# Kernel optimization log

Measured on AMD Instinct MI355X. Metric: run time of the kernel, lower is better.

## Reference

```python
import jax, jax.numpy as jnp
import numpy as np

B, H, S, E = 1, 32, 2048, 512  # batch, num_heads (also head dim), seq, embed
NEG_INF = -1.0e9


def setup_inputs() -> dict:
    key = jax.random.key(0)
    ks = jax.random.split(key, 9)
    query = jax.random.normal(ks[0], (B, H, S, E), dtype=jnp.float32)
    key_t = jax.random.normal(ks[1], (B, H, S, E), dtype=jnp.float32)
    value = jax.random.normal(ks[2], (B, H, S, E), dtype=jnp.float32)
    mask = jax.random.randint(ks[3], (1, 1, S, S), 0, 2).astype(jnp.bool_)
    # Linear(E -> H) weights, torch layout [out, in]
    lim = 1.0 / np.sqrt(E)
    Wq = jax.random.uniform(ks[4], (H, E), jnp.float32, -lim, lim)
    Wk = jax.random.uniform(ks[5], (H, E), jnp.float32, -lim, lim)
    Wv = jax.random.uniform(ks[6], (H, E), jnp.float32, -lim, lim)
    bq = jnp.zeros((H,), jnp.float32)
    bk = jnp.zeros((H,), jnp.float32)
    bv = jnp.zeros((H,), jnp.float32)
    # learned per-head inverse scale; kept away from 0 (torch init of zeros would divide-by-zero)
    inv_scale = jax.random.uniform(ks[7], (1, H, 1, 1), jnp.float32, 0.5, 1.5)
    return {"query": query, "key": key_t, "value": value, "mask": mask,
            "Wq": Wq, "bq": bq, "Wk": Wk, "bk": bk, "Wv": Wv, "bv": bv,
            "inv_scale": inv_scale}


def reference(query, key, value, mask, Wq, bq, Wk, bk, Wv, bv, inv_scale):
    # projections: [B,H,S,E] @ [E,Hd] -> [B,H,S,Hd] with Hd == num_heads
    q = jnp.einsum('bhse,de->bhsd', query, Wq) + bq
    k = jnp.einsum('bhse,de->bhsd', key, Wk) + bk
    v = jnp.einsum('bhse,de->bhsd', value, Wv) + bv
    qk = jnp.einsum('bhsd,bhtd->bhst', q, k)        # [B,H,S,S]
    scaled = qk / inv_scale                          # learned per-head scale
    masked = jnp.where(mask, NEG_INF, scaled)        # custom mask-fill
    attn = jax.nn.softmax(masked, axis=-1)
    # dropout_p = 0.0 -> identity
    out = jnp.einsum('bhst,bhtd->bhsd', attn, v)     # [B,H,S,Hd]
    return out
```

## Files before the change

kernel.cpp:

```cpp
#include <hip/hip_runtime.h>

#define Hh 32
#define Ss 2048
#define Ee 512
#define Dd 32
#define MNEG -1.0e9f
#define LOG2E 1.4426950408889634f
#define KV_SPLIT 4
#define KV_LEN (Ss / KV_SPLIT)

typedef __attribute__((ext_vector_type(4))) float f32x4;
typedef __attribute__((ext_vector_type(4))) int i32x4;
typedef __attribute__((ext_vector_type(8))) __bf16 bf16x8;
typedef __attribute__((ext_vector_type(8))) unsigned short ushort8;
typedef __attribute__((ext_vector_type(4))) unsigned short ushort4v;

__device__ inline unsigned short f2bf(float f) {
  union { float f; unsigned u; } x; x.f = f;
  unsigned r = x.u + 0x7fffu + ((x.u >> 16) & 1u);
  return (unsigned short)(r >> 16);
}

__global__ __launch_bounds__(256) void prep_kernel(
    const int* __restrict__ mask, unsigned int* __restrict__ bits,
    const float* __restrict__ Wq, const float* __restrict__ Wk,
    const float* __restrict__ Wv, unsigned short* __restrict__ Wb) {
  int b = (int)blockIdx.x, t = (int)threadIdx.x;
  if (b < 512) {
    int w = b * 256 + t;
    const i32x4* p = (const i32x4*)(mask + (size_t)w * 32);
    unsigned int bs = 0;
    #pragma unroll
    for (int i = 0; i < 8; ++i) {
      i32x4 v = __builtin_nontemporal_load(&p[i]);
      bs |= (v.x ? 1u : 0u) << (4 * i + 0);
      bs |= (v.y ? 1u : 0u) << (4 * i + 1);
      bs |= (v.z ? 1u : 0u) << (4 * i + 2);
      bs |= (v.w ? 1u : 0u) << (4 * i + 3);
    }
    bits[w] = bs;
  } else {
    int i = (b - 512) * 1024 + t * 4;
    const float* src = (i < 16384) ? (Wq + i)
                     : (i < 32768) ? (Wk + (i - 16384)) : (Wv + (i - 32768));
    f32x4 v = *(const f32x4*)src;
    ushort4v o = { f2bf(v.x), f2bf(v.y), f2bf(v.z), f2bf(v.w) };
    *(ushort4v*)(Wb + i) = o;
  }
}

__global__ __launch_bounds__(256) void proj_kernel(
    const float* __restrict__ Xq, const float* __restrict__ Xk,
    const float* __restrict__ Xv, const unsigned short* __restrict__ Wb,
    const float* __restrict__ bq, const float* __restrict__ bk,
    const float* __restrict__ bv, const float* __restrict__ inv_scale,
    unsigned short* __restrict__ Qb, unsigned short* __restrict__ Kb,
    unsigned short* __restrict__ Vtb) {
  __shared__ unsigned short sb[4][2][16 * 64];

  int blk  = (int)blockIdx.x;
  int seg  = blk >> 10;
  int tid  = (int)threadIdx.x;
  int wv   = tid >> 6, lane = tid & 63;
  int g = lane >> 4, li = lane & 15;
  int lr = lane >> 4;
  int lc = lane & 15;
  int R0 = (blk & 1023) * 64;
  int h  = R0 >> 11;
  int s0 = R0 & 2047;

  const float* X    = (seg == 0) ? Xq : (seg == 1) ? Xk : Xv;
  const float* bias = (seg == 0) ? bq : (seg == 1) ? bk : bv;
  const unsigned short* W = Wb + seg * (Dd * Ee);
  const float* xw = X + (size_t)(R0 + wv * 16) * Ee;

  unsigned short (*mybuf)[16 * 64] = sb[wv];

  auto ld = [&](int c, int i) -> f32x4 {
    return __builtin_nontemporal_load(
        (const f32x4*)(xw + (size_t)(4 * i + lr) * Ee + c * 64 + lc * 4));
  };
  auto wr = [&](int buf, int i, f32x4 v) {
    int r = 4 * i + lr;
    int byteoff = (lc * 8) ^ ((r & 7) << 4);
    ushort4v u = { f2bf(v.x), f2bf(v.y), f2bf(v.z), f2bf(v.w) };
    *(ushort4v*)&mybuf[buf][r * 64 + (byteoff >> 1)] = u;
  };
  auto rd = [&](int buf, int half) -> bf16x8 {
    int byteoff = (half * 64 + g * 16) ^ ((li & 7) << 4);
    return __builtin_bit_cast(bf16x8,
        *(const ushort8*)&mybuf[buf][li * 64 + (byteoff >> 1)]);
  };

  f32x4 acc0 = {0.f, 0.f, 0.f, 0.f};
  f32x4 acc1 = {0.f, 0.f, 0.f, 0.f};

  f32x4 A0 = ld(0, 0), A1 = ld(0, 1), A2 = ld(0, 2), A3 = ld(0, 3);
  f32x4 B0 = ld(1, 0), B1 = ld(1, 1), B2 = ld(1, 2), B3 = ld(1, 3);

  #pragma unroll
  for (int c = 0; c < 8; c += 2) {
    wr(0, 0, A0); wr(0, 1, A1); wr(0, 2, A2); wr(0, 3, A3);
    {
      int cn = (c + 2 < 8) ? (c + 2) : 6;
      A0 = ld(cn, 0); A1 = ld(cn, 1); A2 = ld(cn, 2); A3 = ld(cn, 3);
    }
    {
      const unsigned short* wl = W + (size_t)li * Ee + c * 64 + g * 8;
      ushort8 w00 = *(const ushort8*)(wl);
      ushort8 w01 = *(const ushort8*)(wl + 16 * Ee);
      ushort8 w10 = *(const ushort8*)(wl + 32);
      ushort8 w11 = *(const ushort8*)(wl + 16 * Ee + 32);
      bf16x8 a0 = rd(0, 0), a1 = rd(0, 1);
      acc0 = __builtin_amdgcn_mfma_f32_16x16x32_bf16(
          a0, __builtin_bit_cast(bf16x8, w00), acc0, 0, 0, 0);
      acc1 = __builtin_amdgcn_mfma_f32_16x16x32_bf16(
          a0, __builtin_bit_cast(bf16x8, w01), acc1, 0, 0, 0);
      acc0 = __builtin_amdgcn_mfma_f32_16x16x32_bf16(
          a1, __builtin_bit_cast(bf16x8, w10), acc0, 0, 0, 0);
      acc1 = __builtin_amdgcn_mfma_f32_16x16x32_bf16(
          a1, __builtin_bit_cast(bf16x8, w11), acc1, 0, 0, 0);
    }
    wr(1, 0, B0); wr(1, 1, B1); wr(1, 2, B2); wr(1, 3, B3);
    {
      int cn = (c + 3 < 8) ? (c + 3) : 7;
      B0 = ld(cn, 0); B1 = ld(cn, 1); B2 = ld(cn, 2); B3 = ld(cn, 3);
    }
    {
      const unsigned short* wl = W + (size_t)li * Ee + (c + 1) * 64 + g * 8;
      ushort8 w00 = *(const ushort8*)(wl);
      ushort8 w01 = *(const ushort8*)(wl + 16 * Ee);
      ushort8 w10 = *(const ushort8*)(wl + 32);
      ushort8 w11 = *(const ushort8*)(wl + 16 * Ee + 32);
      bf16x8 a0 = rd(1, 0), a1 = rd(1, 1);
      acc0 = __builtin_amdgcn_mfma_f32_16x16x32_bf16(
          a0, __builtin_bit_cast(bf16x8, w00), acc0, 0, 0, 0);
      acc1 = __builtin_amdgcn_mfma_f32_16x16x32_bf16(
          a0, __builtin_bit_cast(bf16x8, w01), acc1, 0, 0, 0);
      acc0 = __builtin_amdgcn_mfma_f32_16x16x32_bf16(
          a1, __builtin_bit_cast(bf16x8, w10), acc0, 0, 0, 0);
      acc1 = __builtin_amdgcn_mfma_f32_16x16x32_bf16(
          a1, __builtin_bit_cast(bf16x8, w11), acc1, 0, 0, 0);
    }
  }

  float blo = bias[li], bhi = bias[li + 16];
  float cs = (seg == 0) ? (LOG2E / inv_scale[h]) : 1.0f;
  int sw = s0 + wv * 16;
  if (seg < 2) {
    unsigned short* ob = ((seg == 0) ? Qb : Kb) +
        (size_t)h * Ss * Dd + (size_t)(sw + 4 * g) * Dd;
    #pragma unroll
    for (int r = 0; r < 4; ++r) {
      ob[r * Dd + li]      = f2bf((acc0[r] + blo) * cs);
      ob[r * Dd + li + 16] = f2bf((acc1[r] + bhi) * cs);
    }
  } else {
    unsigned short* ob = Vtb + (size_t)h * Dd * Ss;
    int s0v = sw + 4 * g;
    int base = (s0v & ~31) + 8 * g + ((s0v & 16) ? 4 : 0);
    #pragma unroll
    for (int r = 0; r < 4; ++r) {
      ob[(size_t)li * Ss + base + r]        = f2bf(acc0[r] + blo);
      ob[(size_t)(li + 16) * Ss + base + r] = f2bf(acc1[r] + bhi);
    }
  }
}

__global__ __launch_bounds__(256) void attn_kernel(
    const unsigned short* __restrict__ Qb, const unsigned short* __restrict__ Kb,
    const unsigned short* __restrict__ Vt, const unsigned int* __restrict__ mbits,
    float* __restrict__ out) {
  __shared__ float sO[KV_SPLIT][2][8][64];
  __shared__ float sM[KV_SPLIT][2][16];
  __shared__ float sL[KV_SPLIT][2][16];

  int bid  = (int)blockIdx.x;
  int slot = (bid & 7) * 256 + (bid >> 3);
  int w    = (int)threadIdx.x >> 6;
  int lane = (int)threadIdx.x & 63;
  int g = lane >> 4, li = lane & 15;
  int h = slot >> 6, qt = slot & 63;
  int q0 = qt << 5;

  const unsigned short* kb  = Kb + (size_t)h * Ss * Dd;
  const unsigned short* vpb = Vt + (size_t)h * Dd * Ss;
  bf16x8 qfA = __builtin_bit_cast(bf16x8,
      *(const ushort8*)(Qb + (size_t)h * Ss * Dd + (size_t)(q0 + li) * Dd + g * 8));
  bf16x8 qfB = __builtin_bit_cast(bf16x8,
      *(const ushort8*)(Qb + (size_t)h * Ss * Dd + (size_t)(q0 + 16 + li) * Dd + g * 8));
  const unsigned int* mrowA = mbits + (size_t)(q0 + li) * (Ss / 32);
  const unsigned int* mrowB = mrowA + 16 * (Ss / 32);
  const unsigned short* vlo = vpb + (size_t)li * Ss + 8 * g;
  const unsigned short* vhi = vpb + (size_t)(li + 16) * Ss + 8 * g;

  f32x4 oloA = {0.f, 0.f, 0.f, 0.f}, ohiA = {0.f, 0.f, 0.f, 0.f};
  f32x4 oloB = {0.f, 0.f, 0.f, 0.f}, ohiB = {0.f, 0.f, 0.f, 0.f};
  float MA = -__builtin_inff(), LpA = 0.f;
  float MB = -__builtin_inff(), LpB = 0.f;

  auto seg = [&](f32x4 stx, f32x4 sty, unsigned int mword, float& M, float& Lp,
                 f32x4& olo, f32x4& ohi, bf16x8 vl, bf16x8 vh) {
    float s[8];
    #pragma unroll
    for (int r = 0; r < 4; ++r) {
      s[r]     = ((mword >> (4 * g + r)) & 1u)      ? MNEG : stx[r];
      s[4 + r] = ((mword >> (16 + 4 * g + r)) & 1u) ? MNEG : sty[r];
    }
    float pmax = fmaxf(fmaxf(fmaxf(s[0], s[1]), s[2]),
                       fmaxf(fmaxf(s[3], s[4]), fmaxf(fmaxf(s[5], s[6]), s[7])));
    if (!__all(pmax <= M + 8.0f)) {
      float rmax = fmaxf(pmax, __shfl_xor(pmax, 16));
      rmax = fmaxf(rmax, __shfl_xor(rmax, 32));
      float Mn = fmaxf(M, rmax);
      float al = __builtin_amdgcn_exp2f(M - Mn);
      M = Mn; Lp *= al;
      #pragma unroll
      for (int r = 0; r < 4; ++r) {
        float ar = __shfl(al, 4 * g + r);
        olo[r] *= ar; ohi[r] *= ar;
      }
    }
    float p[8];
    #pragma unroll
    for (int j = 0; j < 8; ++j) p[j] = __builtin_amdgcn_exp2f(s[j] - M);
    Lp += ((p[0] + p[1]) + (p[2] + p[3])) + ((p[4] + p[5]) + (p[6] + p[7]));
    bf16x8 af;
    #pragma unroll
    for (int j = 0; j < 8; ++j) af[j] = (__bf16)p[j];
    olo = __builtin_amdgcn_mfma_f32_16x16x32_bf16(af, vl, olo, 0, 0, 0);
    ohi = __builtin_amdgcn_mfma_f32_16x16x32_bf16(af, vh, ohi, 0, 0, 0);
  };

  int kbeg = w * KV_LEN, kend = kbeg + KV_LEN;
  for (int kt = kbeg; kt < kend; kt += 64) {
    bf16x8 k0 = __builtin_bit_cast(bf16x8, *(const ushort8*)(kb + (size_t)(kt      + li) * Dd + g * 8));
    bf16x8 k1 = __builtin_bit_cast(bf16x8, *(const ushort8*)(kb + (size_t)(kt + 16 + li) * Dd + g * 8));
    bf16x8 k2 = __builtin_bit_cast(bf16x8, *(const ushort8*)(kb + (size_t)(kt + 32 + li) * Dd + g * 8));
    bf16x8 k3 = __builtin_bit_cast(bf16x8, *(const ushort8*)(kb + (size_t)(kt + 48 + li) * Dd + g * 8));
    bf16x8 v0lo = __builtin_bit_cast(bf16x8, *(const ushort8*)(vlo + kt));
    bf16x8 v0hi = __builtin_bit_cast(bf16x8, *(const ushort8*)(vhi + kt));
    bf16x8 v1lo = __builtin_bit_cast(bf16x8, *(const ushort8*)(vlo + kt + 32));
    bf16x8 v1hi = __builtin_bit_cast(bf16x8, *(const ushort8*)(vhi + kt + 32));
    uint2 mwA = *(const uint2*)(mrowA + (kt >> 5));
    uint2 mwB = *(const uint2*)(mrowB + (kt >> 5));

    f32x4 z = {0.f, 0.f, 0.f, 0.f};
    f32x4 sA0 = __builtin_amdgcn_mfma_f32_16x16x32_bf16(k0, qfA, z, 0, 0, 0);
    f32x4 sA1 = __builtin_amdgcn_mfma_f32_16x16x32_bf16(k1, qfA, z, 0, 0, 0);
    f32x4 sA2 = __builtin_amdgcn_mfma_f32_16x16x32_bf16(k2, qfA, z, 0, 0, 0);
    f32x4 sA3 = __builtin_amdgcn_mfma_f32_16x16x32_bf16(k3, qfA, z, 0, 0, 0);
    f32x4 sB0 = __builtin_amdgcn_mfma_f32_16x16x32_bf16(k0, qfB, z, 0, 0, 0);
    f32x4 sB1 = __builtin_amdgcn_mfma_f32_16x16x32_bf16(k1, qfB, z, 0, 0, 0);
    f32x4 sB2 = __builtin_amdgcn_mfma_f32_16x16x32_bf16(k2, qfB, z, 0, 0, 0);
    f32x4 sB3 = __builtin_amdgcn_mfma_f32_16x16x32_bf16(k3, qfB, z, 0, 0, 0);

    seg(sA0, sA1, mwA.x, MA, LpA, oloA, ohiA, v0lo, v0hi);
    seg(sA2, sA3, mwA.y, MA, LpA, oloA, ohiA, v1lo, v1hi);
    seg(sB0, sB1, mwB.x, MB, LpB, oloB, ohiB, v0lo, v0hi);
    seg(sB2, sB3, mwB.y, MB, LpB, oloB, ohiB, v1lo, v1hi);
  }

  LpA += __shfl_xor(LpA, 16); LpA += __shfl_xor(LpA, 32);
  LpB += __shfl_xor(LpB, 16); LpB += __shfl_xor(LpB, 32);

  if (lane < 16) {
    sM[w][0][lane] = MA; sL[w][0][lane] = LpA;
    sM[w][1][lane] = MB; sL[w][1][lane] = LpB;
  }
  #pragma unroll
  for (int r = 0; r < 4; ++r) {
    sO[w][0][r][lane]     = oloA[r];
    sO[w][0][4 + r][lane] = ohiA[r];
    sO[w][1][r][lane]     = oloB[r];
    sO[w][1][4 + r][lane] = ohiB[r];
  }
  __syncthreads();

  if (w < 2) {
    int hf = w;
    float* ob = out + (size_t)h * Ss * Dd + (size_t)(q0 + hf * 16) * Dd;
    #pragma unroll
    for (int r = 0; r < 4; ++r) {
      int row = 4 * g + r;
      float M0 = sM[0][hf][row], M1 = sM[1][hf][row];
      float M2 = sM[2][hf][row], M3 = sM[3][hf][row];
      float Mg = fmaxf(fmaxf(M0, M1), fmaxf(M2, M3));
      float e0 = __builtin_amdgcn_exp2f(M0 - Mg);
      float e1 = __builtin_amdgcn_exp2f(M1 - Mg);
      float e2 = __builtin_amdgcn_exp2f(M2 - Mg);
      float e3 = __builtin_amdgcn_exp2f(M3 - Mg);
      float den = sL[0][hf][row] * e0 + sL[1][hf][row] * e1 +
                  sL[2][hf][row] * e2 + sL[3][hf][row] * e3;
      float nlo = sO[0][hf][r][lane] * e0 + sO[1][hf][r][lane] * e1 +
                  sO[2][hf][r][lane] * e2 + sO[3][hf][r][lane] * e3;
      float nhi = sO[0][hf][4 + r][lane] * e0 + sO[1][hf][4 + r][lane] * e1 +
                  sO[2][hf][4 + r][lane] * e2 + sO[3][hf][4 + r][lane] * e3;
      float inv = 1.0f / den;
      ob[row * Dd + li]      = nlo * inv;
      ob[row * Dd + li + 16] = nhi * inv;
    }
  }
}

extern "C" void kernel_launch(void* const* d_in, const int* in_sizes, int n_in,
                              void* d_out, int out_size, void* d_ws, size_t ws_size,
                              hipStream_t stream) {
  const float* query = (const float*)d_in[0];
  const float* key   = (const float*)d_in[1];
  const float* value = (const float*)d_in[2];
  const int*   mask  = (const int*)d_in[3];
  const float* Wq = (const float*)d_in[4];
  const float* bq = (const float*)d_in[5];
  const float* Wk = (const float*)d_in[6];
  const float* bk = (const float*)d_in[7];
  const float* Wv = (const float*)d_in[8];
  const float* bv = (const float*)d_in[9];
  const float* inv_scale = (const float*)d_in[10];

  unsigned short* Qb   = (unsigned short*)d_ws;
  unsigned short* Kbuf = Qb + (size_t)Hh * Ss * Dd;
  unsigned short* Vtb  = Kbuf + (size_t)Hh * Ss * Dd;
  unsigned int*   bits = (unsigned int*)(Vtb + (size_t)Hh * Dd * Ss);
  unsigned short* Wb   = (unsigned short*)(bits + (size_t)Ss * Ss / 32);
  float* out = (float*)d_out;

  dim3 blk(256);
  prep_kernel<<<512 + 48, blk, 0, stream>>>(mask, bits, Wq, Wk, Wv, Wb);
  proj_kernel<<<3072, blk, 0, stream>>>(query, key, value, Wb, bq, bk, bv,
                                        inv_scale, Qb, Kbuf, Vtb);
  attn_kernel<<<2048, blk, 0, stream>>>(Qb, Kbuf, Vtb, bits, out);
}
```

Measured before the change: 155.4 us.

## Double query rows per attention block to reuse K/V tiles across 64 rows

```diff
diff --git a/kernel.cpp b/kernel.cpp
--- a/kernel.cpp
+++ b/kernel.cpp
@@ -171,33 +171,40 @@
     const unsigned short* __restrict__ Qb, const unsigned short* __restrict__ Kb,
     const unsigned short* __restrict__ Vt, const unsigned int* __restrict__ mbits,
     float* __restrict__ out) {
-  __shared__ float sO[KV_SPLIT][2][8][64];
-  __shared__ float sM[KV_SPLIT][2][16];
-  __shared__ float sL[KV_SPLIT][2][16];
+  __shared__ float sO[KV_SPLIT][4][8][64];
+  __shared__ float sM[KV_SPLIT][4][16];
+  __shared__ float sL[KV_SPLIT][4][16];
 
   int bid  = (int)blockIdx.x;
-  int slot = (bid & 7) * 256 + (bid >> 3);
+  int slot = (bid & 7) * 128 + (bid >> 3);
   int w    = (int)threadIdx.x >> 6;
   int lane = (int)threadIdx.x & 63;
   int g = lane >> 4, li = lane & 15;
-  int h = slot >> 6, qt = slot & 63;
-  int q0 = qt << 5;
+  int h = slot >> 5, qt = slot & 31;
+  int q0 = qt << 6;
 
   const unsigned short* kb  = Kb + (size_t)h * Ss * Dd;
   const unsigned short* vpb = Vt + (size_t)h * Dd * Ss;
-  bf16x8 qfA = __builtin_bit_cast(bf16x8,
-      *(const ushort8*)(Qb + (size_t)h * Ss * Dd + (size_t)(q0 + li) * Dd + g * 8));
-  bf16x8 qfB = __builtin_bit_cast(bf16x8,
-      *(const ushort8*)(Qb + (size_t)h * Ss * Dd + (size_t)(q0 + 16 + li) * Dd + g * 8));
+  const unsigned short* qrow = Qb + (size_t)h * Ss * Dd + (size_t)(q0 + li) * Dd + g * 8;
+  bf16x8 qfA = __builtin_bit_cast(bf16x8, *(const ushort8*)(qrow));
+  bf16x8 qfB = __builtin_bit_cast(bf16x8, *(const ushort8*)(qrow + 16 * Dd));
+  bf16x8 qfC = __builtin_bit_cast(bf16x8, *(const ushort8*)(qrow + 32 * Dd));
+  bf16x8 qfD = __builtin_bit_cast(bf16x8, *(const ushort8*)(qrow + 48 * Dd));
   const unsigned int* mrowA = mbits + (size_t)(q0 + li) * (Ss / 32);
   const unsigned int* mrowB = mrowA + 16 * (Ss / 32);
+  const unsigned int* mrowC = mrowA + 32 * (Ss / 32);
+  const unsigned int* mrowD = mrowA + 48 * (Ss / 32);
   const unsigned short* vlo = vpb + (size_t)li * Ss + 8 * g;
   const unsigned short* vhi = vpb + (size_t)(li + 16) * Ss + 8 * g;
 
-  f32x4 oloA = {0.f, 0.f, 0.f, 0.f}, ohiA = {0.f, 0.f, 0.f, 0.f};
-  f32x4 oloB = {0.f, 0.f, 0.f, 0.f}, ohiB = {0.f, 0.f, 0.f, 0.f};
+  f32x4 oloA = {0.f,0.f,0.f,0.f}, ohiA = {0.f,0.f,0.f,0.f};
+  f32x4 oloB = {0.f,0.f,0.f,0.f}, ohiB = {0.f,0.f,0.f,0.f};
+  f32x4 oloC = {0.f,0.f,0.f,0.f}, ohiC = {0.f,0.f,0.f,0.f};
+  f32x4 oloD = {0.f,0.f,0.f,0.f}, ohiD = {0.f,0.f,0.f,0.f};
   float MA = -__builtin_inff(), LpA = 0.f;
   float MB = -__builtin_inff(), LpB = 0.f;
+  float MC = -__builtin_inff(), LpC = 0.f;
+  float MD = -__builtin_inff(), LpD = 0.f;
 
   auto seg = [&](f32x4 stx, f32x4 sty, unsigned int mword, float& M, float& Lp,
                  f32x4& olo, f32x4& ohi, bf16x8 vl, bf16x8 vh) {
@@ -244,29 +251,54 @@
     bf16x8 v1hi = __builtin_bit_cast(bf16x8, *(const ushort8*)(vhi + kt + 32));
     uint2 mwA = *(const uint2*)(mrowA + (kt >> 5));
     uint2 mwB = *(const uint2*)(mrowB + (kt >> 5));
+    uint2 mwC = *(const uint2*)(mrowC + (kt >> 5));
+    uint2 mwD = *(const uint2*)(mrowD + (kt >> 5));
 
     f32x4 z = {0.f, 0.f, 0.f, 0.f};
-    f32x4 sA0 = __builtin_amdgcn_mfma_f32_16x16x32_bf16(k0, qfA, z, 0, 0, 0);
-    f32x4 sA1 = __builtin_amdgcn_mfma_f32_16x16x32_bf16(k1, qfA, z, 0, 0, 0);
-    f32x4 sA2 = __builtin_amdgcn_mfma_f32_16x16x32_bf16(k2, qfA, z, 0, 0, 0);
-    f32x4 sA3 = __builtin_amdgcn_mfma_f32_16x16x32_bf16(k3, qfA, z, 0, 0, 0);
-    f32x4 sB0 = __builtin_amdgcn_mfma_f32_16x16x32_bf16(k0, qfB, z, 0, 0, 0);
-    f32x4 sB1 = __builtin_amdgcn_mfma_f32_16x16x32_bf16(k1, qfB, z, 0, 0, 0);
-    f32x4 sB2 = __builtin_amdgcn_mfma_f32_16x16x32_bf16(k2, qfB, z, 0, 0, 0);
-    f32x4 sB3 = __builtin_amdgcn_mfma_f32_16x16x32_bf16(k3, qfB, z, 0, 0, 0);
-
-    seg(sA0, sA1, mwA.x, MA, LpA, oloA, ohiA, v0lo, v0hi);
-    seg(sA2, sA3, mwA.y, MA, LpA, oloA, ohiA, v1lo, v1hi);
-    seg(sB0, sB1, mwB.x, MB, LpB, oloB, ohiB, v0lo, v0hi);
-    seg(sB2, sB3, mwB.y, MB, LpB, oloB, ohiB, v1lo, v1hi);
+    {
+      f32x4 s0 = __builtin_amdgcn_mfma_f32_16x16x32_bf16(k0, qfA, z, 0, 0, 0);
+      f32x4 s1 = __builtin_amdgcn_mfma_f32_16x16x32_bf16(k1, qfA, z, 0, 0, 0);
+      f32x4 s2 = __builtin_amdgcn_mfma_f32_16x16x32_bf16(k2, qfA, z, 0, 0, 0);
+      f32x4 s3 = __builtin_amdgcn_mfma_f32_16x16x32_bf16(k3, qfA, z, 0, 0, 0);
+      seg(s0, s1, mwA.x, MA, LpA, oloA, ohiA, v0lo, v0hi);
+      seg(s2, s3, mwA.y, MA, LpA, oloA, ohiA, v1lo, v1hi);
+    }
+    {
+      f32x4 s0 = __builtin_amdgcn_mfma_f32_16x16x32_bf16(k0, qfB, z, 0, 0, 0);
+      f32x4 s1 = __builtin_amdgcn_mfma_f32_16x16x32_bf16(k1, qfB, z, 0, 0, 0);
+      f32x4 s2 = __builtin_amdgcn_mfma_f32_16x16x32_bf16(k2, qfB, z, 0, 0, 0);
+      f32x4 s3 = __builtin_amdgcn_mfma_f32_16x16x32_bf16(k3, qfB, z, 0, 0, 0);
+      seg(s0, s1, mwB.x, MB, LpB, oloB, ohiB, v0lo, v0hi);
+      seg(s2, s3, mwB.y, MB, LpB, oloB, ohiB, v1lo, v1hi);
+    }
+    {
+      f32x4 s0 = __builtin_amdgcn_mfma_f32_16x16x32_bf16(k0, qfC, z, 0, 0, 0);
+      f32x4 s1 = __builtin_amdgcn_mfma_f32_16x16x32_bf16(k1, qfC, z, 0, 0, 0);
+      f32x4 s2 = __builtin_amdgcn_mfma_f32_16x16x32_bf16(k2, qfC, z, 0, 0, 0);
+      f32x4 s3 = __builtin_amdgcn_mfma_f32_16x16x32_bf16(k3, qfC, z, 0, 0, 0);
+      seg(s0, s1, mwC.x, MC, LpC, oloC, ohiC, v0lo, v0hi);
+      seg(s2, s3, mwC.y, MC, LpC, oloC, ohiC, v1lo, v1hi);
+    }
+    {
+      f32x4 s0 = __builtin_amdgcn_mfma_f32_16x16x32_bf16(k0, qfD, z, 0, 0, 0);
+      f32x4 s1 = __builtin_amdgcn_mfma_f32_16x16x32_bf16(k1, qfD, z, 0, 0, 0);
+      f32x4 s2 = __builtin_amdgcn_mfma_f32_16x16x32_bf16(k2, qfD, z, 0, 0, 0);
+      f32x4 s3 = __builtin_amdgcn_mfma_f32_16x16x32_bf16(k3, qfD, z, 0, 0, 0);
+      seg(s0, s1, mwD.x, MD, LpD, oloD, ohiD, v0lo, v0hi);
+      seg(s2, s3, mwD.y, MD, LpD, oloD, ohiD, v1lo, v1hi);
+    }
   }
 
   LpA += __shfl_xor(LpA, 16); LpA += __shfl_xor(LpA, 32);
   LpB += __shfl_xor(LpB, 16); LpB += __shfl_xor(LpB, 32);
+  LpC += __shfl_xor(LpC, 16); LpC += __shfl_xor(LpC, 32);
+  LpD += __shfl_xor(LpD, 16); LpD += __shfl_xor(LpD, 32);
 
   if (lane < 16) {
     sM[w][0][lane] = MA; sL[w][0][lane] = LpA;
     sM[w][1][lane] = MB; sL[w][1][lane] = LpB;
+    sM[w][2][lane] = MC; sL[w][2][lane] = LpC;
+    sM[w][3][lane] = MD; sL[w][3][lane] = LpD;
   }
   #pragma unroll
   for (int r = 0; r < 4; ++r) {
@@ -274,10 +306,14 @@
     sO[w][0][4 + r][lane] = ohiA[r];
     sO[w][1][r][lane]     = oloB[r];
     sO[w][1][4 + r][lane] = ohiB[r];
+    sO[w][2][r][lane]     = oloC[r];
+    sO[w][2][4 + r][lane] = ohiC[r];
+    sO[w][3][r][lane]     = oloD[r];
+    sO[w][3][4 + r][lane] = ohiD[r];
   }
   __syncthreads();
 
-  if (w < 2) {
+  {
     int hf = w;
     float* ob = out + (size_t)h * Ss * Dd + (size_t)(q0 + hf * 16) * Dd;
     #pragma unroll
@@ -329,5 +365,5 @@
   prep_kernel<<<512 + 48, blk, 0, stream>>>(mask, bits, Wq, Wk, Wv, Wb);
   proj_kernel<<<3072, blk, 0, stream>>>(query, key, value, Wb, bq, bk, bv,
                                         inv_scale, Qb, Kbuf, Vtb);
-  attn_kernel<<<2048, blk, 0, stream>>>(Qb, Kbuf, Vtb, bits, out);
-}
+  attn_kernel<<<1024, blk, 0, stream>>>(Qb, Kbuf, Vtb, bits, out);
+}
```

Result: faster. 144.3 us (-7.1%).
